# Kernel optimization log

Measured on AMD Instinct MI355X. Metric: run time of the kernel, lower is better.

The kernel has to match this reference:

```python
import jax, jax.numpy as jnp
import numpy as np

N = 32768   # nodes
E = 32768   # edges
ND, ED, GD = 12, 5, 11
H = 64
T = 4
STEPS = 3


def setup_inputs() -> dict:
    key = jax.random.key(0)
    ks = jax.random.split(key, 24)
    s = 0.05
    p = lambda k, sh: (jax.random.normal(k, sh) * s).astype(jnp.float32)
    return dict(
        x=jax.random.normal(ks[0], (N, ND), jnp.float32),
        edge_index=jax.random.randint(ks[1], (2, E), 0, N, jnp.int64),
        edge_attr=jax.random.uniform(ks[2], (E, ED), jnp.float32),
        u=jax.random.normal(ks[3], (1, GD), jnp.float32),
        Wp=p(ks[4], (H, ND + GD)), bp=p(ks[5], (H,)),
        We1=p(ks[6], (H, ED)), be1=p(ks[7], (H,)),
        We2=p(ks[8], (H * H, H)), be2=p(ks[9], (H * H,)),
        root=p(ks[10], (H, H)), conv_b=p(ks[11], (H,)),
        Wih=p(ks[12], (3 * H, H)), bih=p(ks[13], (3 * H,)),
        Whh=p(ks[14], (3 * H, H)), bhh=p(ks[15], (3 * H,)),
        Wd1=p(ks[16], (H, 2 * H + ED)), bd1=p(ks[17], (H,)),
        Wd2=p(ks[18], (H // 2, H)), bd2=p(ks[19], (H // 2,)),
        Wd3=p(ks[20], (T, H // 2)), bd3=p(ks[21], (T,)),
    )


def _forward(x, edge_index, edge_attr, u,
             Wp, bp, We1, be1, We2, be2, root, conv_b,
             Wih, bih, Whh, bhh, Wd1, bd1, Wd2, bd2, Wd3, bd3):
    n = x.shape[0]
    e = edge_attr.shape[0]
    src, dst = edge_index[0], edge_index[1]

    # input projection with broadcast global features (batch=None path)
    u_node = jnp.broadcast_to(u, (n, u.shape[-1]))
    h = jnp.tanh(jnp.concatenate([x, u_node], axis=-1) @ Wp.T + bp)

    # edge MLP -> per-edge (H,H) weight matrices; edge_attr is loop-invariant
    ew = jax.nn.relu(edge_attr @ We1.T + be1) @ We2.T + be2   # (E, H*H)
    ew = ew.reshape(e, H, H)                                   # (E, H, H)

    # mean-aggregation denominators (clamped to 1 like scatter-mean)
    counts = jnp.clip(jax.ops.segment_sum(jnp.ones((e,), h.dtype), dst, num_segments=n), 1.0)

    for _ in range(STEPS):
        # NNConv: gather src features, per-edge matmul, scatter-mean into dst
        msg = jnp.einsum('eh,eho->eo', h[src], ew)             # (E, H)
        agg = jax.ops.segment_sum(msg, dst, num_segments=n) / counts[:, None]
        m = jax.nn.relu(agg + h @ root + conv_b)               # dropout off (eval)
        # GRUCell (torch gate order: r, z, n)
        gi = m @ Wih.T + bih
        gh = h @ Whh.T + bhh
        r = jax.nn.sigmoid(gi[:, :H] + gh[:, :H])
        z = jax.nn.sigmoid(gi[:, H:2 * H] + gh[:, H:2 * H])
        ng = jnp.tanh(gi[:, 2 * H:] + r * gh[:, 2 * H:])
        h = (1.0 - z) * ng + z * h

    # per-edge decoder
    e_in = jnp.concatenate([h[src], h[dst], edge_attr], axis=-1)
    d = jax.nn.relu(e_in @ Wd1.T + bd1)
    d = jax.nn.relu(d @ Wd2.T + bd2)
    return d @ Wd3.T + bd3                                     # (E, T)


def reference(x, edge_index, edge_attr, u,
              Wp, bp, We1, be1, We2, be2, root, conv_b,
              Wih, bih, Whh, bhh, Wd1, bd1, Wd2, bd2, Wd3, bd3):
    return _forward(x, edge_index, edge_attr, u,
                    Wp, bp, We1, be1, We2, be2, root, conv_b,
                    Wih, bih, Whh, bhh, Wd1, bd1, Wd2, bd2, Wd3, bd3)
```

## Files before the change

### kernel.cpp

```cpp
#include <hip/hip_runtime.h>
#include <hip/hip_bf16.h>
#include <stdint.h>


#define N_NODES 32768
#define N_EDGES 32768
#define STEPS 3

typedef __attribute__((ext_vector_type(8))) short short8;
typedef __attribute__((ext_vector_type(4))) float float4v;

__device__ __forceinline__ float bf2f(unsigned short u) {
    union { unsigned int i; float f; } v; v.i = ((unsigned int)u) << 16; return v.f;
}
__device__ __forceinline__ unsigned short f2bf(float f) {
    union { float f; unsigned int i; } v; v.f = f;
    unsigned int x = v.i;
    return (unsigned short)((x + 0x7fffu + ((x >> 16) & 1u)) >> 16);
}
__device__ __forceinline__ unsigned int fbits(float f) {
    union { float f; unsigned int i; } v; v.f = f; return v.i;
}

__device__ __forceinline__ short8 packA(float hv, const float* hf) {
    union { short8 v; unsigned int u[4]; } r;
#pragma unroll
    for (int p = 0; p < 4; p++) {
        unsigned int p0 = fbits(hv * hf[2 * p]) + 0x8000u;
        unsigned int p1 = fbits(hv * hf[2 * p + 1]) + 0x8000u;
        r.u[p] = __builtin_amdgcn_perm(p1, p0, 0x07060302u);
    }
    return r.v;
}

__device__ __forceinline__ void gload_lds16(const void* g, void* l) {
    __builtin_amdgcn_global_load_lds(
        (__attribute__((address_space(1))) void*)g,
        (__attribute__((address_space(3))) void*)l, 16, 0, 0);
}

__global__ __launch_bounds__(256) void k_setup(
    const float* __restrict__ root, const float* __restrict__ Wih,
    const float* __restrict__ Whh,
    const float* __restrict__ We2, const float* __restrict__ be2,
    const float* __restrict__ Wd1, const float* __restrict__ bd1,
    const float* __restrict__ Wd2,
    const float* __restrict__ x, const float* __restrict__ u,
    const float* __restrict__ Wp, const float* __restrict__ bp,
    const float* __restrict__ ea, const float* __restrict__ We1,
    const float* __restrict__ be1,
    unsigned short* __restrict__ rootTf, unsigned short* __restrict__ wcombf,
    unsigned short* __restrict__ w2tf,
    unsigned short* __restrict__ wd1f, unsigned short* __restrict__ wd2f,
    float* __restrict__ h, unsigned short* __restrict__ hb,
    unsigned short* __restrict__ hid, float* __restrict__ aggcnt)
{
    int b = blockIdx.x, tid = threadIdx.x;
    if (b < 144) {
        int i = b * 256 + tid;
        if (i < 4096) {
            int j = i & 7, lane = (i >> 3) & 63, g = i >> 9;
            int kb = g >> 2, nf = g & 3;
            int o = nf * 16 + (lane & 15);
            int k = kb * 32 + (lane >> 4) * 8 + j;
            rootTf[i] = f2bf(root[k * 64 + o]);
        } else if (i < 4096 + 32768) {
            int t = i - 4096;
            int j = t & 7, lane = (t >> 3) & 63, g = t >> 9;
            int kb = g >> 4, nf = g & 15;
            int cp = nf * 16 + (lane & 15);
            int k = kb * 32 + (lane >> 4) * 8 + j;
            float v;
            if (cp < 128)      v = (k < 64) ? Wih[cp * 64 + k] : Whh[cp * 64 + (k - 64)];
            else if (cp < 192) v = (k < 64) ? Wih[cp * 64 + k] : 0.f;
            else               v = (k < 64) ? 0.f : Whh[(cp - 64) * 64 + (k - 64)];
            wcombf[t] = f2bf(v);
        }
    } else if (b < 1184) {
        int t = (b - 144) * 256 + tid;
        if (t < 65 * 4096) {
            int kk = t >> 12, r = t & 4095;
            int j = r & 7, lane = (r >> 3) & 63, g = r >> 9;
            int half = g >> 2, nf = g & 3;
            int o = nf * 16 + (lane & 15);
            int hh = half * 32 + (lane >> 4) * 8 + j;
            float v = (kk < 64) ? We2[((size_t)(hh * 64 + o)) * 64 + kk]
                                : be2[(size_t)hh * 64 + o];
            w2tf[t] = f2bf(v);
        }
    } else if (b < 1232) {
        int i = (b - 1184) * 256 + tid;
        if (i < 10240) {
            int j = i & 7, lane = (i >> 3) & 63, g = i >> 9;
            int kb = g >> 2, nf = g & 3;
            int o = nf * 16 + (lane & 15);
            int k = kb * 32 + (lane >> 4) * 8 + j;
            float v = (k < 133) ? Wd1[(size_t)o * 133 + k] : (k == 133 ? bd1[o] : 0.f);
            wd1f[i] = f2bf(v);
        } else if (i < 10240 + 2048) {
            int t = i - 10240;
            int j = t & 7, lane = (t >> 3) & 63, g = t >> 9;
            int kb = g >> 1, nf = g & 1;
            int o = nf * 16 + (lane & 15);
            int k = kb * 32 + (lane >> 4) * 8 + j;
            wd2f[t] = f2bf(Wd2[(size_t)o * 64 + k]);
        }
    } else if (b < 9424) {
        int idx = (b - 1232) * 256 + tid;
        int n = idx >> 6, j = idx & 63;
        const float* wr = Wp + j * 23;
        const float* xr = x + (size_t)n * 12;
        float s = bp[j];
#pragma unroll
        for (int i = 0; i < 12; i++) s += xr[i] * wr[i];
#pragma unroll
        for (int i = 0; i < 11; i++) s += u[i] * wr[12 + i];
        float v = tanhf(s);
        h[idx] = v; hb[idx] = f2bf(v);
    } else if (b < 17616) {
        int idx = (b - 9424) * 256 + tid;
        int e = idx >> 6, j = idx & 63;
        float s = be1[j];
#pragma unroll
        for (int i = 0; i < 5; i++) s += ea[(size_t)e * 5 + i] * We1[j * 5 + i];
        hid[idx] = f2bf(s > 0.f ? s : 0.f);
    } else {
        int idx = (b - 17616) * 1024 + tid * 4;
        if (idx < 2129920) {
            float4v z = {0.f, 0.f, 0.f, 0.f};
            *(float4v*)(aggcnt + idx) = z;
        }
    }
}

__global__ __launch_bounds__(256) void k_counts(
    const int* __restrict__ ei, float* __restrict__ counts)
{
    int i = blockIdx.x * 256 + threadIdx.x;
    if (i < N_EDGES) atomicAdd(&counts[ei[N_EDGES + i]], 1.0f);
}

__global__ __launch_bounds__(512) void k_msg_fused(
    const unsigned short* __restrict__ hid,
    const unsigned short* __restrict__ hb,
    const unsigned short* __restrict__ w2tf,
    const int* __restrict__ ei,
    float* __restrict__ agg)
{
    __shared__ unsigned short buf[2][2][4096];
    int tid = threadIdx.x, wave = tid >> 6, lane = tid & 63;
    int l15 = lane & 15, quad = lane >> 4;
    int mf = wave & 3, kh = wave >> 2;
    int ebase = blockIdx.x * 64 + mf * 16;
    int e_a = ebase + l15;
    int src = ei[e_a];

    union { short8 v[4]; unsigned short u[32]; } hrow;
#pragma unroll
    for (int i = 0; i < 4; i++)
        hrow.v[i] = *(const short8*)(hid + (size_t)e_a * 64 + kh * 32 + i * 8);

    float hf0[8], hf1[8];
    {
        short8 h0 = *(const short8*)(hb + (size_t)src * 64 + quad * 8);
        short8 h1 = *(const short8*)(hb + (size_t)src * 64 + 32 + quad * 8);
#pragma unroll
        for (int j = 0; j < 8; j++) {
            hf0[j] = bf2f((unsigned short)h0[j]);
            hf1[j] = bf2f((unsigned short)h1[j]);
        }
    }

    auto stage = [&](int kkv, int db) {
        const unsigned short* g = w2tf + (size_t)kkv * 4096;
#pragma unroll
        for (int c = 0; c < 2; c++) {
            int chunk = mf * 2 + c;
            gload_lds16(g + (size_t)chunk * 512 + lane * 8, &buf[kh][db][chunk * 512]);
        }
    };

    int kk0 = kh ? 32 : 0;
    stage(kk0, 0);

    float4v acc[4] = {};
    int cur = 0;
#pragma unroll
    for (int i = 0; i <= 32; i++) {
        __syncthreads();
        if ((kh == 0 && i + 1 < 32) || (kh == 1 && i + 1 <= 32))
            stage(kk0 + i + 1, cur ^ 1);
        bool active = (kh == 1) || (i < 32);
        if (active) {
            float hv = (kh && i == 32) ? 1.0f : bf2f(hrow.u[i & 31]);
            short8 a0 = packA(hv, hf0);
            short8 a1 = packA(hv, hf1);
            const unsigned short* bp = &buf[kh][cur][0];
#pragma unroll
            for (int nf = 0; nf < 4; nf++) {
                short8 b0 = *(const short8*)(bp + (0 * 4 + nf) * 512 + lane * 8);
                acc[nf] = __builtin_amdgcn_mfma_f32_16x16x32_bf16(a0, b0, acc[nf], 0, 0, 0);
            }
#pragma unroll
            for (int nf = 0; nf < 4; nf++) {
                short8 b1 = *(const short8*)(bp + (1 * 4 + nf) * 512 + lane * 8);
                acc[nf] = __builtin_amdgcn_mfma_f32_16x16x32_bf16(a1, b1, acc[nf], 0, 0, 0);
            }
        }
        cur ^= 1;
    }

    __syncthreads();
    float* mg = (float*)&buf[0][0][0];
    if (kh == 1) {
#pragma unroll
        for (int nf = 0; nf < 4; nf++)
#pragma unroll
            for (int r = 0; r < 4; r++)
                mg[mf * 1024 + lane * 16 + nf * 4 + r] = acc[nf][r];
    }
    __syncthreads();
    if (kh == 0) {
        int dsts[4];
#pragma unroll
        for (int r = 0; r < 4; r++) dsts[r] = ei[N_EDGES + ebase + quad * 4 + r];
#pragma unroll
        for (int nf = 0; nf < 4; nf++)
#pragma unroll
            for (int r = 0; r < 4; r++)
                atomicAdd(agg + (size_t)dsts[r] * 64 + nf * 16 + l15,
                          acc[nf][r] + mg[mf * 1024 + lane * 16 + nf * 4 + r]);
    }
}

__global__ __launch_bounds__(256) void k_node(
    const unsigned short* __restrict__ hb_in,
    const unsigned short* __restrict__ rootTf,
    const unsigned short* __restrict__ wcombf,
    float* __restrict__ agg, const float* __restrict__ counts,
    const float* __restrict__ conv_b,
    const float* __restrict__ bih, const float* __restrict__ bhh,
    float* __restrict__ h, unsigned short* __restrict__ hb_out)
{
    __shared__ unsigned short m_lds[64 * 72];
    int tid = threadIdx.x, w = tid >> 6, lane = tid & 63;
    int l15 = lane & 15, quad = lane >> 4;
    int node0 = blockIdx.x * 64;
    int row0 = w * 16;

    float4v acc1[4] = {};
    {
        short8 a1[2];
#pragma unroll
        for (int kb = 0; kb < 2; kb++)
            a1[kb] = *(const short8*)(hb_in + (size_t)(node0 + row0 + l15) * 64 + kb * 32 + quad * 8);
#pragma unroll
        for (int kb = 0; kb < 2; kb++)
#pragma unroll
            for (int nf = 0; nf < 4; nf++) {
                short8 b = *(const short8*)(rootTf + (size_t)((kb * 4 + nf) * 64 + lane) * 8);
                acc1[nf] = __builtin_amdgcn_mfma_f32_16x16x32_bf16(a1[kb], b, acc1[nf], 0, 0, 0);
            }
    }
#pragma unroll
    for (int rr = 0; rr < 4; rr++) {
        int nl = row0 + quad * 4 + rr;
        float cnt = counts[node0 + nl]; if (cnt < 1.f) cnt = 1.f;
        float rcp = 1.f / cnt;
#pragma unroll
        for (int nf = 0; nf < 4; nf++) {
            int c = nf * 16 + l15;
            float* ap = agg + (size_t)(node0 + nl) * 64 + c;
            float av = *ap;
            *ap = 0.f;
            float mv = av * rcp + acc1[nf][rr] + conv_b[c];
            m_lds[nl * 72 + c] = f2bf(mv > 0.f ? mv : 0.f);
        }
    }
    __syncthreads();

    float4v acc2[16] = {};
#pragma unroll
    for (int kb = 0; kb < 4; kb++) {
        short8 a2;
        if (kb < 2)
            a2 = *(const short8*)(m_lds + (row0 + l15) * 72 + kb * 32 + quad * 8);
        else
            a2 = *(const short8*)(hb_in + (size_t)(node0 + row0 + l15) * 64 + (kb - 2) * 32 + quad * 8);
#pragma unroll
        for (int nf = 0; nf < 16; nf++) {
            short8 b = *(const short8*)(wcombf + (size_t)((kb * 16 + nf) * 64 + lane) * 8);
            acc2[nf] = __builtin_amdgcn_mfma_f32_16x16x32_bf16(a2, b, acc2[nf], 0, 0, 0);
        }
    }

#pragma unroll
    for (int nf0 = 0; nf0 < 4; nf0++) {
        int c = nf0 * 16 + l15;
        float br = bih[c] + bhh[c];
        float bz = bih[64 + c] + bhh[64 + c];
        float bni = bih[128 + c], bnh = bhh[128 + c];
#pragma unroll
        for (int rr = 0; rr < 4; rr++) {
            int node = node0 + row0 + quad * 4 + rr;
            float gr = 1.f / (1.f + __expf(-(acc2[nf0][rr] + br)));
            float gz = 1.f / (1.f + __expf(-(acc2[nf0 + 4][rr] + bz)));
            float ng = tanhf(acc2[nf0 + 8][rr] + bni + gr * (acc2[nf0 + 12][rr] + bnh));
            float ho = h[(size_t)node * 64 + c];
            float hn = (1.f - gz) * ng + gz * ho;
            h[(size_t)node * 64 + c] = hn;
            hb_out[(size_t)node * 64 + c] = f2bf(hn);
        }
    }
}

__global__ __launch_bounds__(256) void k_decoder(
    const unsigned short* __restrict__ hb, const int* __restrict__ ei,
    const float* __restrict__ ea,
    const unsigned short* __restrict__ wd1f, const unsigned short* __restrict__ wd2f,
    const float* __restrict__ bd2,
    const float* __restrict__ Wd3, const float* __restrict__ bd3,
    float* __restrict__ out)
{
    __shared__ unsigned short d1f[4][1024];
    __shared__ float d2s[4][16 * 33];
    int tid = threadIdx.x, w = tid >> 6, lane = tid & 63;
    int l15 = lane & 15, quad = lane >> 4;
    int ebase = blockIdx.x * 64 + w * 16;
    int e = ebase + l15;
    int src = ei[e], dst = ei[N_EDGES + e];

    short8 a[5];
#pragma unroll
    for (int kb = 0; kb < 2; kb++) {
        a[kb]     = *(const short8*)(hb + (size_t)src * 64 + kb * 32 + quad * 8);
        a[2 + kb] = *(const short8*)(hb + (size_t)dst * 64 + kb * 32 + quad * 8);
    }
    {
        union { short8 v; unsigned short u[8]; } tea;
#pragma unroll
        for (int j = 0; j < 8; j++) {
            float vv = 0.f;
            if (quad == 0) vv = (j < 5) ? ea[(size_t)e * 5 + j] : (j == 5 ? 1.f : 0.f);
            tea.u[j] = f2bf(vv);
        }
        a[4] = tea.v;
    }

    float4v acc1[4] = {};
#pragma unroll
    for (int kb = 0; kb < 5; kb++)
#pragma unroll
        for (int nf = 0; nf < 4; nf++) {
            short8 b = *(const short8*)(wd1f + (size_t)((kb * 4 + nf) * 64 + lane) * 8);
            acc1[nf] = __builtin_amdgcn_mfma_f32_16x16x32_bf16(a[kb], b, acc1[nf], 0, 0, 0);
        }
#pragma unroll
    for (int nf = 0; nf < 4; nf++) {
        int kbp = nf >> 1;
        int lanep_hi = ((nf & 1) * 2 + (l15 >> 3)) * 16;
        int jp = l15 & 7;
#pragma unroll
        for (int r = 0; r < 4; r++) {
            float v = acc1[nf][r];
            d1f[w][kbp * 512 + (lanep_hi + quad * 4 + r) * 8 + jp] = f2bf(v > 0.f ? v : 0.f);
        }
    }
    float4v acc2[2] = {};
#pragma unroll
    for (int kb = 0; kb < 2; kb++) {
        short8 a2 = *(const short8*)(&d1f[w][kb * 512 + lane * 8]);
#pragma unroll
        for (int nf = 0; nf < 2; nf++) {
            short8 b = *(const short8*)(wd2f + (size_t)((kb * 2 + nf) * 64 + lane) * 8);
            acc2[nf] = __builtin_amdgcn_mfma_f32_16x16x32_bf16(a2, b, acc2[nf], 0, 0, 0);
        }
    }
#pragma unroll
    for (int nf = 0; nf < 2; nf++) {
        int c = nf * 16 + l15;
        float bias = bd2[c];
#pragma unroll
        for (int r = 0; r < 4; r++) {
            float v = acc2[nf][r] + bias;
            d2s[w][(quad * 4 + r) * 33 + c] = v > 0.f ? v : 0.f;
        }
    }
    {
        int e_l = lane >> 2, t = lane & 3;
        float s = bd3[t];
        const float* w3 = Wd3 + t * 32;
        const float* dr = &d2s[w][e_l * 33];
#pragma unroll
        for (int k = 0; k < 32; k++) s += w3[k] * dr[k];
        out[(size_t)(ebase + e_l) * 4 + t] = s;
    }
}

extern "C" void kernel_launch(void* const* d_in, const int* in_sizes, int n_in,
                              void* d_out, int out_size, void* d_ws, size_t ws_size,
                              hipStream_t stream)
{
    const float* x      = (const float*)d_in[0];
    const int*   ei     = (const int*)d_in[1];
    const float* ea     = (const float*)d_in[2];
    const float* u      = (const float*)d_in[3];
    const float* Wp     = (const float*)d_in[4];
    const float* bp     = (const float*)d_in[5];
    const float* We1    = (const float*)d_in[6];
    const float* be1    = (const float*)d_in[7];
    const float* We2    = (const float*)d_in[8];
    const float* be2    = (const float*)d_in[9];
    const float* root   = (const float*)d_in[10];
    const float* conv_b = (const float*)d_in[11];
    const float* Wih    = (const float*)d_in[12];
    const float* bih    = (const float*)d_in[13];
    const float* Whh    = (const float*)d_in[14];
    const float* bhh    = (const float*)d_in[15];
    const float* Wd1    = (const float*)d_in[16];
    const float* bd1    = (const float*)d_in[17];
    const float* Wd2    = (const float*)d_in[18];
    const float* bd2    = (const float*)d_in[19];
    const float* Wd3    = (const float*)d_in[20];
    const float* bd3    = (const float*)d_in[21];
    float* out = (float*)d_out;

    char* ws = (char*)d_ws;
    size_t off = 0;
    auto take = [&](size_t bytes) -> char* {
        char* p = ws + off; off = (off + bytes + 255) & ~(size_t)255; return p;
    };
    float*          h      = (float*)take((size_t)N_NODES * 64 * 4);
    unsigned short* hb     = (unsigned short*)take((size_t)N_NODES * 64 * 2);
    unsigned short* hid    = (unsigned short*)take((size_t)N_EDGES * 64 * 2);
    float*          aggcnt = (float*)take((size_t)(N_NODES * 64 + N_NODES) * 4);
    float*          agg    = aggcnt;
    float*          cnts   = aggcnt + (size_t)N_NODES * 64;
    unsigned short* w2tf   = (unsigned short*)take((size_t)65 * 4096 * 2);
    unsigned short* rootTf = (unsigned short*)take((size_t)4096 * 2);
    unsigned short* wcombf = (unsigned short*)take((size_t)32768 * 2);
    unsigned short* wd1f   = (unsigned short*)take((size_t)10240 * 2);
    unsigned short* wd2f   = (unsigned short*)take((size_t)2048 * 2);
    (void)ws_size;

    k_setup<<<19696, 256, 0, stream>>>(root, Wih, Whh, We2, be2, Wd1, bd1, Wd2,
                                       x, u, Wp, bp, ea, We1, be1,
                                       rootTf, wcombf, w2tf, wd1f, wd2f,
                                       h, hb, hid, aggcnt);
    k_counts<<<128, 256, 0, stream>>>(ei, cnts);

    for (int s = 0; s < STEPS; s++) {
        k_msg_fused<<<N_EDGES / 64, 512, 0, stream>>>(hid, hb, w2tf, ei, agg);
        k_node<<<N_NODES / 64, 256, 0, stream>>>(hb, rootTf, wcombf, agg, cnts,
                                                 conv_b, bih, bhh, h, hb);
    }
    k_decoder<<<N_EDGES / 64, 256, 0, stream>>>(hb, ei, ea, wd1f, wd2f, bd2,
                                                Wd3, bd3, out);
}
```

Measured before the change: 297.0 us.

## Stage two weight slices per barrier and drop fp32 hidden-state buffer

The message kernel now stages two 4096-element weight slices per double-buffer phase, which halves the number of barrier iterations, and adds a min-blocks hint to the launch bounds. The fp32 copy of the hidden state is removed; the GRU blend reads the previous state from the bf16 buffer, which cuts memory traffic but adds rounding error. The weight workspace is padded to 66 slices because the last pair reads one slice past the original end. LDS per block doubles, which may reduce occupancy.

After: 267.0 us. -10.1%, faster.

```diff
diff --git a/kernel.cpp b/kernel.cpp
--- a/kernel.cpp
+++ b/kernel.cpp
@@ -52,7 +52,7 @@
     unsigned short* __restrict__ rootTf, unsigned short* __restrict__ wcombf,
     unsigned short* __restrict__ w2tf,
     unsigned short* __restrict__ wd1f, unsigned short* __restrict__ wd2f,
-    float* __restrict__ h, unsigned short* __restrict__ hb,
+    unsigned short* __restrict__ hb,
     unsigned short* __restrict__ hid, float* __restrict__ aggcnt)
 {
     int b = blockIdx.x, tid = threadIdx.x;
@@ -115,8 +115,7 @@
         for (int i = 0; i < 12; i++) s += xr[i] * wr[i];
 #pragma unroll
         for (int i = 0; i < 11; i++) s += u[i] * wr[12 + i];
-        float v = tanhf(s);
-        h[idx] = v; hb[idx] = f2bf(v);
+        hb[idx] = f2bf(tanhf(s));
     } else if (b < 17616) {
         int idx = (b - 9424) * 256 + tid;
         int e = idx >> 6, j = idx & 63;
@@ -140,14 +139,14 @@
     if (i < N_EDGES) atomicAdd(&counts[ei[N_EDGES + i]], 1.0f);
 }
 
-__global__ __launch_bounds__(512) void k_msg_fused(
+__global__ __launch_bounds__(512, 4) void k_msg_fused(
     const unsigned short* __restrict__ hid,
     const unsigned short* __restrict__ hb,
     const unsigned short* __restrict__ w2tf,
     const int* __restrict__ ei,
     float* __restrict__ agg)
 {
-    __shared__ unsigned short buf[2][2][4096];
+    __shared__ unsigned short buf[2][2][8192];
     int tid = threadIdx.x, wave = tid >> 6, lane = tid & 63;
     int l15 = lane & 15, quad = lane >> 4;
     int mf = wave & 3, kh = wave >> 2;
@@ -171,31 +170,31 @@
         }
     }
 
-    auto stage = [&](int kkv, int db) {
-        const unsigned short* g = w2tf + (size_t)kkv * 4096;
-#pragma unroll
-        for (int c = 0; c < 2; c++) {
-            int chunk = mf * 2 + c;
+    int kk0 = kh ? 32 : 0;
+    auto stage = [&](int pair, int db) {
+        const unsigned short* g = w2tf + (size_t)(kk0 + 2 * pair) * 4096;
+#pragma unroll
+        for (int c = 0; c < 4; c++) {
+            int chunk = mf * 4 + c;
             gload_lds16(g + (size_t)chunk * 512 + lane * 8, &buf[kh][db][chunk * 512]);
         }
     };
 
-    int kk0 = kh ? 32 : 0;
-    stage(kk0, 0);
+    stage(0, 0);
 
     float4v acc[4] = {};
     int cur = 0;
 #pragma unroll
-    for (int i = 0; i <= 32; i++) {
+    for (int i = 0; i <= 16; i++) {
         __syncthreads();
-        if ((kh == 0 && i + 1 < 32) || (kh == 1 && i + 1 <= 32))
-            stage(kk0 + i + 1, cur ^ 1);
-        bool active = (kh == 1) || (i < 32);
-        if (active) {
-            float hv = (kh && i == 32) ? 1.0f : bf2f(hrow.u[i & 31]);
+        if ((kh == 0 && i + 1 < 16) || (kh == 1 && i + 1 <= 16))
+            stage(i + 1, cur ^ 1);
+        int nkk = (kh == 0) ? (i < 16 ? 2 : 0) : (i < 16 ? 2 : 1);
+        for (int s = 0; s < nkk; s++) {
+            float hv = (kh == 1 && i == 16) ? 1.0f : bf2f(hrow.u[2 * i + s]);
             short8 a0 = packA(hv, hf0);
             short8 a1 = packA(hv, hf1);
-            const unsigned short* bp = &buf[kh][cur][0];
+            const unsigned short* bp = &buf[kh][cur][s * 4096];
 #pragma unroll
             for (int nf = 0; nf < 4; nf++) {
                 short8 b0 = *(const short8*)(bp + (0 * 4 + nf) * 512 + lane * 8);
@@ -240,7 +239,7 @@
     float* __restrict__ agg, const float* __restrict__ counts,
     const float* __restrict__ conv_b,
     const float* __restrict__ bih, const float* __restrict__ bhh,
-    float* __restrict__ h, unsigned short* __restrict__ hb_out)
+    unsigned short* __restrict__ hb_out)
 {
     __shared__ unsigned short m_lds[64 * 72];
     int tid = threadIdx.x, w = tid >> 6, lane = tid & 63;
@@ -306,9 +305,8 @@
             float gr = 1.f / (1.f + __expf(-(acc2[nf0][rr] + br)));
             float gz = 1.f / (1.f + __expf(-(acc2[nf0 + 4][rr] + bz)));
             float ng = tanhf(acc2[nf0 + 8][rr] + bni + gr * (acc2[nf0 + 12][rr] + bnh));
-            float ho = h[(size_t)node * 64 + c];
+            float ho = bf2f(hb_in[(size_t)node * 64 + c]);
             float hn = (1.f - gz) * ng + gz * ho;
-            h[(size_t)node * 64 + c] = hn;
             hb_out[(size_t)node * 64 + c] = f2bf(hn);
         }
     }
@@ -430,13 +428,12 @@
     auto take = [&](size_t bytes) -> char* {
         char* p = ws + off; off = (off + bytes + 255) & ~(size_t)255; return p;
     };
-    float*          h      = (float*)take((size_t)N_NODES * 64 * 4);
     unsigned short* hb     = (unsigned short*)take((size_t)N_NODES * 64 * 2);
     unsigned short* hid    = (unsigned short*)take((size_t)N_EDGES * 64 * 2);
     float*          aggcnt = (float*)take((size_t)(N_NODES * 64 + N_NODES) * 4);
     float*          agg    = aggcnt;
     float*          cnts   = aggcnt + (size_t)N_NODES * 64;
-    unsigned short* w2tf   = (unsigned short*)take((size_t)65 * 4096 * 2);
+    unsigned short* w2tf   = (unsigned short*)take((size_t)66 * 4096 * 2);
     unsigned short* rootTf = (unsigned short*)take((size_t)4096 * 2);
     unsigned short* wcombf = (unsigned short*)take((size_t)32768 * 2);
     unsigned short* wd1f   = (unsigned short*)take((size_t)10240 * 2);
@@ -446,13 +443,13 @@
     k_setup<<<19696, 256, 0, stream>>>(root, Wih, Whh, We2, be2, Wd1, bd1, Wd2,
                                        x, u, Wp, bp, ea, We1, be1,
                                        rootTf, wcombf, w2tf, wd1f, wd2f,
-                                       h, hb, hid, aggcnt);
+                                       hb, hid, aggcnt);
     k_counts<<<128, 256, 0, stream>>>(ei, cnts);
 
     for (int s = 0; s < STEPS; s++) {
         k_msg_fused<<<N_EDGES / 64, 512, 0, stream>>>(hid, hb, w2tf, ei, agg);
         k_node<<<N_NODES / 64, 256, 0, stream>>>(hb, rootTf, wcombf, agg, cnts,
-                                                 conv_b, bih, bhh, h, hb);
+                                                 conv_b, bih, bhh, hb);
     }
     k_decoder<<<N_EDGES / 64, 256, 0, stream>>>(hb, ei, ea, wd1f, wd2f, bd2,
                                                 Wd3, bd3, out);
```
